# Optimization experiments

Hardware: AMD Instinct MI355X
Metric: run time of the kernel (lower is better)

The kernel has to match this reference:

```python
import jax, jax.numpy as jnp
import numpy as np

L, D, OC, GROUPS, EPS = 256, 1280, 128, 8, 1e-5


def setup_inputs() -> dict:
    key = jax.random.key(0)
    k1, k2 = jax.random.split(key)
    feats = jax.random.normal(k1, (L, D), dtype=jnp.float32)
    # Conv2d(3d, out_ch, kernel_size=1) weight flattened to (out_ch, 3d)
    W = jax.random.normal(k2, (OC, 3 * D), dtype=jnp.float32) * (1.0 / np.sqrt(3 * D))
    b = jnp.zeros((OC,), dtype=jnp.float32)
    gamma = jnp.ones((OC,), dtype=jnp.float32)
    beta = jnp.zeros((OC,), dtype=jnp.float32)
    return {"feats": feats, "W": W, "b": b, "gamma": gamma, "beta": beta}


def reference(feats, W, b, gamma, beta):
    fi = feats[:, None, :]                     # (L, 1, d)
    fj = feats[None, :, :]                     # (1, L, d)
    add = fi + fj                              # (L, L, d)
    diff = jnp.abs(fi - fj)                    # (L, L, d)
    had = fi * fj                              # (L, L, d)
    pair = jnp.concatenate([add, diff, had], axis=-1)  # (L, L, 3d)
    # 1x1 conv == per-pixel linear: (L, L, 3d) x (out_ch, 3d)^T -> (L, L, out_ch)
    x = jnp.einsum('ijc,oc->ijo', pair, W) + b
    # GroupNorm(8, out_ch) on batch=1: normalize over (C/g, L, L) per group
    xg = jnp.transpose(x, (2, 0, 1)).reshape(GROUPS, OC // GROUPS, L, L)
    mean = jnp.mean(xg, axis=(1, 2, 3), keepdims=True)
    var = jnp.var(xg, axis=(1, 2, 3), keepdims=True)
    xn = ((xg - mean) * jax.lax.rsqrt(var + EPS)).reshape(OC, L, L)
    xn = xn * gamma[:, None, None] + beta[:, None, None]
    out = jax.nn.gelu(xn, approximate=False)   # torch nn.GELU default = exact erf
    return out[None]                           # (1, out_ch, L, L)
```

## Files before the change

kernel.cpp:

```cpp
#include <hip/hip_runtime.h>
#include <math.h>

typedef unsigned int uint;
typedef unsigned short ushort;

typedef __attribute__((ext_vector_type(8))) __bf16 bf16x8;
typedef __attribute__((ext_vector_type(16))) float floatx16;

#define NFEAT 327680
#define NW    491520

union U4B8 { uint4 u; bf16x8 b; };

__device__ inline ushort f2b(float f) {
  uint u = __float_as_uint(f);
  u += 0x7fffu + ((u >> 16) & 1u);
  return (ushort)(u >> 16);
}
__device__ inline float blo(uint u) { return __uint_as_float(u << 16); }
__device__ inline float bhi(uint u) { return __uint_as_float(u & 0xffff0000u); }

#if __has_builtin(__builtin_amdgcn_cvt_pk_bf16_f32)
typedef __attribute__((ext_vector_type(2))) __bf16 bf16x2;
__device__ inline uint cvtpk(float a, float b) {
  bf16x2 r = __builtin_amdgcn_cvt_pk_bf16_f32(a, b);
  return *(uint*)&r;
}
__device__ inline uint cvtpk_abs(float a, float b) { return cvtpk(fabsf(a), fabsf(b)); }
#else
__device__ inline uint cvtpk(float a, float b) {
  uint au = __float_as_uint(a) + 0x8000u;
  uint bu = __float_as_uint(b) + 0x8000u;
  return __builtin_amdgcn_perm(bu, au, 0x07060302u);
}
__device__ inline uint cvtpk_abs(float a, float b) { return cvtpk(a, b) & 0x7fff7fffu; }
#endif

__device__ inline void async16(const ushort* g, ushort* l) {
  __builtin_amdgcn_global_load_lds((const __attribute__((address_space(1))) uint*)g,
                                   (__attribute__((address_space(3))) uint*)l, 16, 0, 0);
}

__global__ void prep_kernel(const float* __restrict__ feats,
                            const float* __restrict__ W,
                            ushort* __restrict__ fB,
                            ushort* __restrict__ wB,
                            float* __restrict__ stats,
                            float* __restrict__ Aoi) {
  int idx = blockIdx.x * 256 + threadIdx.x;
  if (blockIdx.x == 0 && threadIdx.x < 16) stats[threadIdx.x] = 0.0f;
  if (idx < 32768) Aoi[idx] = 0.0f;
  if (idx < NFEAT) fB[idx] = f2b(feats[idx]);
  else             wB[idx - NFEAT] = f2b(W[idx - NFEAT]);
}

__global__ __launch_bounds__(256, 2) void gemma_kernel(
    const ushort* __restrict__ fB, const ushort* __restrict__ wB,
    float* __restrict__ Aoi) {
  __shared__ float red[4][4096];
  const int tid = threadIdx.x, lane = tid & 63, w = tid >> 6;
  const int i0 = (blockIdx.x >> 2) << 5;
  const int kq = blockIdx.x & 3;
  const int rr = lane & 31, half = lane >> 5;
  floatx16 a4[4];
  #pragma unroll
  for (int ot = 0; ot < 4; ++ot)
    #pragma unroll
    for (int r = 0; r < 16; ++r) a4[ot][r] = 0.0f;
  const int kbase = kq * 320 + w * 80 + half * 8;
  #pragma unroll
  for (int ks = 0; ks < 5; ++ks) {
    const int k = kbase + ks * 16;
    U4B8 bf; bf.u = *(const uint4*)(fB + (i0 + rr) * 1280 + k);
    #pragma unroll
    for (int ot = 0; ot < 4; ++ot) {
      U4B8 af; af.u = *(const uint4*)(wB + (ot * 32 + rr) * 3840 + k);
      a4[ot] = __builtin_amdgcn_mfma_f32_32x32x16_bf16(af.b, bf.b, a4[ot], 0, 0, 0);
    }
  }
  #pragma unroll
  for (int ot = 0; ot < 4; ++ot)
    #pragma unroll
    for (int r = 0; r < 16; ++r) {
      const int orow = (r & 3) + 8 * (r >> 2) + 4 * half;
      red[w][(ot * 32 + orow) * 32 + rr] = a4[ot][r];
    }
  __syncthreads();
  for (int e = tid; e < 4096; e += 256) {
    float s = red[0][e] + red[1][e] + red[2][e] + red[3][e];
    atomicAdd(&Aoi[(e >> 5) * 256 + i0 + (e & 31)], s);
  }
}

__device__ inline void build(const uint4 vj, const float fi8[8], U4B8& d, U4B8& h) {
  uint ju[4] = {vj.x, vj.y, vj.z, vj.w};
  uint* pd = &d.u.x; uint* ph = &h.u.x;
  #pragma unroll
  for (int t = 0; t < 4; ++t) {
    float j0f = blo(ju[t]), j1f = bhi(ju[t]);
    float i0 = fi8[2 * t], i1 = fi8[2 * t + 1];
    pd[t] = cvtpk_abs(i0 - j0f, i1 - j1f);
    ph[t] = cvtpk(i0 * j0f, i1 * j1f);
  }
}

__global__ __launch_bounds__(256, 5) void gemm_kernel(
    const ushort* __restrict__ fB, const ushort* __restrict__ wB,
    const float* __restrict__ bias, const float* __restrict__ Aoi,
    float* __restrict__ xout, float* __restrict__ stats) {
  __shared__ __align__(16) ushort Wl[2 * 128 * 64];

  const int tid = threadIdx.x;
  const int blk = blockIdx.x;
  const int i_row = blk >> 2;
  const int j0 = (blk & 3) << 6;
  const int lane = tid & 63;
  const int w = tid >> 6;
  const int wo = (w >> 1) << 6;
  const int wm = (w & 1) << 5;
  const int rr = lane & 31;
  const int half = lane >> 5;
  const int rr7 = lane & 7;

  const ushort* gsrc[4];
  #pragma unroll
  for (int p = 0; p < 4; ++p) {
    const int seg = w * 4 + p;
    const int row = seg * 8 + (lane >> 3);
    const int g = (lane & 7) ^ (lane >> 3);
    gsrc[p] = wB + row * 3840 + 1280 + (g >> 2) * 1280 + (g & 3) * 8;
  }

  const ushort* fip = fB + i_row * 1280 + half * 8;
  const ushort* fjp = fB + (j0 + wm + rr) * 1280 + half * 8;

  floatx16 acc[2];
  #pragma unroll
  for (int a = 0; a < 2; ++a)
    #pragma unroll
    for (int r = 0; r < 16; ++r) acc[a][r] = 0.0f;

  #pragma unroll
  for (int p = 0; p < 4; ++p)
    async16(gsrc[p], &Wl[(w * 4 + p) * 512]);
  uint4 vi[2], vj[2];
  #pragma unroll
  for (int st = 0; st < 2; ++st) {
    vi[st] = *(const uint4*)(fip + st * 16);
    vj[st] = *(const uint4*)(fjp + st * 16);
  }
  __syncthreads();

  for (int cc = 0; cc < 40; ++cc) {
    const ushort* Wc = &Wl[(cc & 1) * 8192];
    uint4 vin[2], vjn[2];
    if (cc < 39) {
      const int cn = (cc + 1) << 5;
      #pragma unroll
      for (int p = 0; p < 4; ++p)
        async16(gsrc[p] + cn, &Wl[((cc & 1) ^ 1) * 8192 + (w * 4 + p) * 512]);
      __builtin_amdgcn_sched_barrier(0);
      #pragma unroll
      for (int st = 0; st < 2; ++st) {
        vin[st] = *(const uint4*)(fip + cn + st * 16);
        vjn[st] = *(const uint4*)(fjp + cn + st * 16);
      }
      __builtin_amdgcn_sched_barrier(0);
    }
    #pragma unroll
    for (int st = 0; st < 2; ++st) {
      float fi8[8];
      {
        uint iu[4] = {vi[st].x, vi[st].y, vi[st].z, vi[st].w};
        #pragma unroll
        for (int t = 0; t < 4; ++t) { fi8[2*t] = blo(iu[t]); fi8[2*t+1] = bhi(iu[t]); }
      }
      U4B8 dfr, hfr;
      build(vj[st], fi8, dfr, hfr);
      const int g0 = (st << 1) + half;
      #pragma unroll
      for (int ot = 0; ot < 2; ++ot) {
        const int rowb = (wo + ot * 32 + rr) << 6;
        bf16x8 ad = *(const bf16x8*)(Wc + rowb + ((g0 ^ rr7) << 3));
        bf16x8 ah = *(const bf16x8*)(Wc + rowb + (((g0 + 4) ^ rr7) << 3));
        acc[ot] = __builtin_amdgcn_mfma_f32_32x32x16_bf16(ad, dfr.b, acc[ot], 0, 0, 0);
        acc[ot] = __builtin_amdgcn_mfma_f32_32x32x16_bf16(ah, hfr.b, acc[ot], 0, 0, 0);
      }
    }
    if (cc < 39) {
      __builtin_amdgcn_sched_barrier(0);
      __builtin_amdgcn_s_waitcnt(0x0F74);
      __builtin_amdgcn_s_barrier();
      __builtin_amdgcn_sched_barrier(0);
      __asm__ volatile("" ::: "memory");
      #pragma unroll
      for (int st = 0; st < 2; ++st) { vi[st] = vin[st]; vj[st] = vjn[st]; }
    }
  }

  float gs[2][2] = {{0.f, 0.f}, {0.f, 0.f}};
  float gq[2][2] = {{0.f, 0.f}, {0.f, 0.f}};
  const int jg = j0 + wm + rr;
  const int mglob = i_row * 256 + jg;
  #pragma unroll
  for (int ot = 0; ot < 2; ++ot) {
    #pragma unroll
    for (int r = 0; r < 16; ++r) {
      const int orow = (r & 3) + 8 * (r >> 2) + 4 * half;
      const int o = wo + ot * 32 + orow;
      float x = acc[ot][r] + Aoi[o * 256 + i_row] + Aoi[o * 256 + jg] + bias[o];
      xout[o * 65536 + mglob] = x;
      gs[ot][r >> 3] += x;
      gq[ot][r >> 3] += x * x;
    }
  }
  __syncthreads();
  float* sred = (float*)Wl;
  if (tid < 16) sred[tid] = 0.0f;
  __syncthreads();
  #pragma unroll
  for (int ot = 0; ot < 2; ++ot) {
    #pragma unroll
    for (int rg = 0; rg < 2; ++rg) {
      float s = gs[ot][rg], qv = gq[ot][rg];
      for (int off = 32; off > 0; off >>= 1) {
        s += __shfl_xor(s, off, 64);
        qv += __shfl_xor(qv, off, 64);
      }
      if (lane == 0) {
        const int g = (wo >> 4) + ot * 2 + rg;
        atomicAdd(&sred[g], s);
        atomicAdd(&sred[8 + g], qv);
      }
    }
  }
  __syncthreads();
  if (tid < 16) atomicAdd(&stats[tid], sred[tid]);
}

__global__ void norm_kernel(float* __restrict__ xout,
                            const float* __restrict__ stats,
                            const float* __restrict__ gamma,
                            const float* __restrict__ beta) {
  const int idx = blockIdx.x * 256 + threadIdx.x;
  const int e = idx << 2;
  const int o = e >> 16;
  const int g = o >> 4;
  const float invN = 1.0f / 1048576.0f;
  const float mean = stats[g] * invN;
  const float var = stats[8 + g] * invN - mean * mean;
  const float inv = rsqrtf(var + 1e-5f);
  const float ga = gamma[o], be = beta[o];
  float4 v = *(float4*)(xout + e);
  float* pv = &v.x;
  #pragma unroll
  for (int t = 0; t < 4; ++t) {
    float xn = (pv[t] - mean) * inv * ga + be;
    pv[t] = 0.5f * xn * (1.0f + erff(xn * 0.70710678118654752f));
  }
  *(float4*)(xout + e) = v;
}

extern "C" void kernel_launch(void* const* d_in, const int* in_sizes, int n_in,
                              void* d_out, int out_size, void* d_ws, size_t ws_size,
                              hipStream_t stream) {
  const float* feats = (const float*)d_in[0];
  const float* W     = (const float*)d_in[1];
  const float* bias  = (const float*)d_in[2];
  const float* gamma = (const float*)d_in[3];
  const float* beta  = (const float*)d_in[4];
  float* out = (float*)d_out;

  ushort* fB = (ushort*)d_ws;
  ushort* wB = fB + NFEAT;
  float* stats = (float*)(wB + NW);
  float* Aoi = stats + 16;

  prep_kernel<<<3200, 256, 0, stream>>>(feats, W, fB, wB, stats, Aoi);
  gemma_kernel<<<32, 256, 0, stream>>>(fB, wB, Aoi);
  gemm_kernel<<<1024, 256, 0, stream>>>(fB, wB, bias, Aoi, out, stats);
  norm_kernel<<<8192, 256, 0, stream>>>(out, stats, gamma, beta);
}
```

Before: 179.5 us.

## Pre-swizzle W into MFMA fragment layout and load directly to registers

Adds a pass in the prep kernel that writes the diff/hadamard parts of W as bf16 pairs arranged in per-lane MFMA A-fragment order. The GEMM kernel then reads its weight fragments straight from global memory (via cache) into registers, dropping the LDS double buffer, the async global-to-LDS copies, and the per-iteration waitcnt and block barrier. This removes LDS traffic and synchronisation, but each block now re-reads weights from L2 with no sharing across waves. It also adds register pressure, so launch bounds drop from 5 to 4.

After: 383.7 us. 2.14x slower.

```diff
diff --git a/kernel.cpp b/kernel.cpp
--- a/kernel.cpp
+++ b/kernel.cpp
@@ -9,6 +9,7 @@
 
 #define NFEAT 327680
 #define NW    491520
+#define NWT   327680
 
 union U4B8 { uint4 u; bf16x8 b; };
 
@@ -36,22 +37,30 @@
 __device__ inline uint cvtpk_abs(float a, float b) { return cvtpk(a, b) & 0x7fff7fffu; }
 #endif
 
-__device__ inline void async16(const ushort* g, ushort* l) {
-  __builtin_amdgcn_global_load_lds((const __attribute__((address_space(1))) uint*)g,
-                                   (__attribute__((address_space(3))) uint*)l, 16, 0, 0);
-}
-
 __global__ void prep_kernel(const float* __restrict__ feats,
                             const float* __restrict__ W,
                             ushort* __restrict__ fB,
                             ushort* __restrict__ wB,
                             float* __restrict__ stats,
-                            float* __restrict__ Aoi) {
+                            float* __restrict__ Aoi,
+                            uint* __restrict__ Wt) {
   int idx = blockIdx.x * 256 + threadIdx.x;
   if (blockIdx.x == 0 && threadIdx.x < 16) stats[threadIdx.x] = 0.0f;
   if (idx < 32768) Aoi[idx] = 0.0f;
-  if (idx < NFEAT) fB[idx] = f2b(feats[idx]);
-  else             wB[idx - NFEAT] = f2b(W[idx - NFEAT]);
+  if (idx < NFEAT) {
+    fB[idx] = f2b(feats[idx]);
+  } else if (idx < NFEAT + NW) {
+    wB[idx - NFEAT] = f2b(W[idx - NFEAT]);
+  } else {
+    const uint u = idx - (NFEAT + NW);
+    const uint frag = u >> 8, q = u & 255;
+    const uint rg = frag & 3, term = (frag >> 2) & 1, st = (frag >> 3) & 1, cc = frag >> 4;
+    const uint l = q >> 2, t = q & 3;
+    const uint row = rg * 32 + (l & 31);
+    const uint k = cc * 32 + st * 16 + (l >> 5) * 8 + t * 2;
+    const float* src = W + row * 3840 + 1280 + term * 1280 + k;
+    Wt[u] = (uint)f2b(src[0]) | ((uint)f2b(src[1]) << 16);
+  }
 }
 
 __global__ __launch_bounds__(256, 2) void gemma_kernel(
@@ -104,11 +113,11 @@
   }
 }
 
-__global__ __launch_bounds__(256, 5) void gemm_kernel(
-    const ushort* __restrict__ fB, const ushort* __restrict__ wB,
+__global__ __launch_bounds__(256, 4) void gemm_kernel(
+    const ushort* __restrict__ fB, const uint* __restrict__ Wt,
     const float* __restrict__ bias, const float* __restrict__ Aoi,
     float* __restrict__ xout, float* __restrict__ stats) {
-  __shared__ __align__(16) ushort Wl[2 * 128 * 64];
+  __shared__ float sred[16];
 
   const int tid = threadIdx.x;
   const int blk = blockIdx.x;
@@ -120,16 +129,14 @@
   const int wm = (w & 1) << 5;
   const int rr = lane & 31;
   const int half = lane >> 5;
-  const int rr7 = lane & 7;
-
-  const ushort* gsrc[4];
-  #pragma unroll
-  for (int p = 0; p < 4; ++p) {
-    const int seg = w * 4 + p;
-    const int row = seg * 8 + (lane >> 3);
-    const int g = (lane & 7) ^ (lane >> 3);
-    gsrc[p] = wB + row * 3840 + 1280 + (g >> 2) * 1280 + (g & 3) * 8;
-  }
+  const int rg0 = wo >> 5;
+
+  const uint* pw[2][2];
+  #pragma unroll
+  for (int st = 0; st < 2; ++st)
+    #pragma unroll
+    for (int term = 0; term < 2; ++term)
+      pw[st][term] = Wt + (st * 8 + term * 4 + rg0) * 256 + lane * 4;
 
   const ushort* fip = fB + i_row * 1280 + half * 8;
   const ushort* fjp = fB + (j0 + wm + rr) * 1280 + half * 8;
@@ -140,32 +147,31 @@
     #pragma unroll
     for (int r = 0; r < 16; ++r) acc[a][r] = 0.0f;
 
-  #pragma unroll
-  for (int p = 0; p < 4; ++p)
-    async16(gsrc[p], &Wl[(w * 4 + p) * 512]);
   uint4 vi[2], vj[2];
   #pragma unroll
   for (int st = 0; st < 2; ++st) {
     vi[st] = *(const uint4*)(fip + st * 16);
     vj[st] = *(const uint4*)(fjp + st * 16);
   }
-  __syncthreads();
 
   for (int cc = 0; cc < 40; ++cc) {
-    const ushort* Wc = &Wl[(cc & 1) * 8192];
+    uint4 wf[2][2][2];
+    #pragma unroll
+    for (int st = 0; st < 2; ++st)
+      #pragma unroll
+      for (int term = 0; term < 2; ++term) {
+        wf[st][term][0] = *(const uint4*)(pw[st][term]);
+        wf[st][term][1] = *(const uint4*)(pw[st][term] + 256);
+        pw[st][term] += 4096;
+      }
     uint4 vin[2], vjn[2];
     if (cc < 39) {
       const int cn = (cc + 1) << 5;
       #pragma unroll
-      for (int p = 0; p < 4; ++p)
-        async16(gsrc[p] + cn, &Wl[((cc & 1) ^ 1) * 8192 + (w * 4 + p) * 512]);
-      __builtin_amdgcn_sched_barrier(0);
-      #pragma unroll
       for (int st = 0; st < 2; ++st) {
         vin[st] = *(const uint4*)(fip + cn + st * 16);
         vjn[st] = *(const uint4*)(fjp + cn + st * 16);
       }
-      __builtin_amdgcn_sched_barrier(0);
     }
     #pragma unroll
     for (int st = 0; st < 2; ++st) {
@@ -177,22 +183,16 @@
       }
       U4B8 dfr, hfr;
       build(vj[st], fi8, dfr, hfr);
-      const int g0 = (st << 1) + half;
       #pragma unroll
       for (int ot = 0; ot < 2; ++ot) {
-        const int rowb = (wo + ot * 32 + rr) << 6;
-        bf16x8 ad = *(const bf16x8*)(Wc + rowb + ((g0 ^ rr7) << 3));
-        bf16x8 ah = *(const bf16x8*)(Wc + rowb + (((g0 + 4) ^ rr7) << 3));
-        acc[ot] = __builtin_amdgcn_mfma_f32_32x32x16_bf16(ad, dfr.b, acc[ot], 0, 0, 0);
-        acc[ot] = __builtin_amdgcn_mfma_f32_32x32x16_bf16(ah, hfr.b, acc[ot], 0, 0, 0);
+        U4B8 ad, ah;
+        ad.u = wf[st][0][ot];
+        ah.u = wf[st][1][ot];
+        acc[ot] = __builtin_amdgcn_mfma_f32_32x32x16_bf16(ad.b, dfr.b, acc[ot], 0, 0, 0);
+        acc[ot] = __builtin_amdgcn_mfma_f32_32x32x16_bf16(ah.b, hfr.b, acc[ot], 0, 0, 0);
       }
     }
     if (cc < 39) {
-      __builtin_amdgcn_sched_barrier(0);
-      __builtin_amdgcn_s_waitcnt(0x0F74);
-      __builtin_amdgcn_s_barrier();
-      __builtin_amdgcn_sched_barrier(0);
-      __asm__ volatile("" ::: "memory");
       #pragma unroll
       for (int st = 0; st < 2; ++st) { vi[st] = vin[st]; vj[st] = vjn[st]; }
     }
@@ -214,8 +214,6 @@
       gq[ot][r >> 3] += x * x;
     }
   }
-  __syncthreads();
-  float* sred = (float*)Wl;
   if (tid < 16) sred[tid] = 0.0f;
   __syncthreads();
   #pragma unroll
@@ -275,9 +273,10 @@
   ushort* wB = fB + NFEAT;
   float* stats = (float*)(wB + NW);
   float* Aoi = stats + 16;
-
-  prep_kernel<<<3200, 256, 0, stream>>>(feats, W, fB, wB, stats, Aoi);
+  uint* Wt = (uint*)(Aoi + 32768);
+
+  prep_kernel<<<4480, 256, 0, stream>>>(feats, W, fB, wB, stats, Aoi, Wt);
   gemma_kernel<<<32, 256, 0, stream>>>(fB, wB, Aoi);
-  gemm_kernel<<<1024, 256, 0, stream>>>(fB, wB, bias, Aoi, out, stats);
+  gemm_kernel<<<1024, 256, 0, stream>>>(fB, Wt, bias, Aoi, out, stats);
   norm_kernel<<<8192, 256, 0, stream>>>(out, stats, gamma, beta);
 }
```
